# Optimization experiments

Measured on AMD Instinct MI355X. Metric: run time of the kernel, lower is better.

The kernel has to match this reference:

```python
import jax, jax.numpy as jnp
import numpy as np

EPS = 1e-5
LEAK = 0.33  # scn LeakyReLU default leakiness


def leaky(x):
    return jnp.where(x > 0, x, LEAK * x)


def subm_conv(feat, idx, mask, w):
    # feat: [N,C], idx: [N,K] int, mask: [N,K] bool, w: [K,Cin,Cout]
    g = feat[idx] * mask[..., None]          # [N,K,C] gather of active neighbors
    return jnp.einsum('nkc,kcd->nd', g, w)   # [N,Cout]


def batch_norm(x, gamma, beta):
    # scn BatchNormalization in training mode: batch stats over active sites
    m = x.mean(axis=0)
    v = x.var(axis=0)
    return (x - m) * jax.lax.rsqrt(v + EPS) * gamma + beta


def setup_inputs() -> dict:
    key = jax.random.key(0)
    ks = jax.random.split(key, 8)
    N, K, C, B = 131072, 9, 64, 4
    features = jax.random.normal(ks[0], (N, C), dtype=jnp.float32)
    neighbor_idx = jax.random.randint(ks[1], (N, K), 0, N, dtype=jnp.int32)
    # center offset always points at self (submanifold conv semantics)
    neighbor_idx = neighbor_idx.at[:, K // 2].set(jnp.arange(N, dtype=jnp.int32))
    neighbor_mask = jax.random.randint(ks[2], (N, K), 0, 2) > 0
    neighbor_mask = neighbor_mask.at[:, K // 2].set(True)
    scale = 1.0 / np.sqrt(K * C)
    conv1_w = jax.random.normal(ks[3], (B, K, C, C), dtype=jnp.float32) * scale
    conv2_w = jax.random.normal(ks[4], (B, K, C, C), dtype=jnp.float32) * scale
    bn1_gamma = jnp.ones((B, C), dtype=jnp.float32)
    bn1_beta = jnp.zeros((B, C), dtype=jnp.float32)
    bn2_gamma = jnp.ones((B, C), dtype=jnp.float32)
    bn2_beta = jnp.zeros((B, C), dtype=jnp.float32)
    return {
        'features': features, 'neighbor_idx': neighbor_idx, 'neighbor_mask': neighbor_mask,
        'conv1_w': conv1_w, 'bn1_gamma': bn1_gamma, 'bn1_beta': bn1_beta,
        'conv2_w': conv2_w, 'bn2_gamma': bn2_gamma, 'bn2_beta': bn2_beta,
    }


def reference(features, neighbor_idx, neighbor_mask, conv1_w, bn1_gamma, bn1_beta,
              conv2_w, bn2_gamma, bn2_beta):
    x = features
    n_blocks = conv1_w.shape[0]
    for b in range(n_blocks):
        residual = x
        out = subm_conv(x, neighbor_idx, neighbor_mask, conv1_w[b])
        out = leaky(batch_norm(out, bn1_gamma[b], bn1_beta[b]))
        out = subm_conv(out, neighbor_idx, neighbor_mask, conv2_w[b])
        out = batch_norm(out, bn2_gamma[b], bn2_beta[b])
        x = leaky(out + residual)
    return x
```

## Files before the change

kernel.cpp:

```cpp
#include <hip/hip_runtime.h>
#include <hip/hip_bf16.h>
#include <stdint.h>

#define NROWS 131072
#define EPSBN 1e-5f
#define LEAKK 0.33f
#define NCOPY 8

typedef __bf16 bf16x8_t __attribute__((ext_vector_type(8)));
typedef float  f32x4_t  __attribute__((ext_vector_type(4)));

__device__ __forceinline__ float leaky_f(float x) { return fmaxf(x, LEAKK * x); }

#define GLDS16(g, l)                                                          \
    __builtin_amdgcn_global_load_lds(                                         \
        (const __attribute__((address_space(1))) void*)(g),                   \
        (__attribute__((address_space(3))) void*)(l), 16, 0, 0)

#define CFENCE() asm volatile("" ::: "memory")

__global__ __launch_bounds__(256, 4) void conv_kernel(
    const __bf16* __restrict__ src,
    const int* __restrict__ cidxT,
    const __bf16* __restrict__ wt,
    __bf16* __restrict__ dst,
    float* __restrict__ stat_out)
{
    __shared__ char Bw[2][8192];

    const int tid  = threadIdx.x;
    const int lane = tid & 63;
    const int wv   = tid >> 6;
    const int quad = lane >> 4;
    const int l15  = lane & 15;
    const int row0 = blockIdx.x << 7;
    const int srow = tid >> 3;
    const int cg   = (tid & 7) ^ (srow & 7);
    const int ldsl = (tid & 192) << 4;
    const int sxor = l15 & 7;

    const char* srcb = (const char*)src;
    const char* wtb  = (const char*)wt;

    f32x4_t acc[2][4];
#pragma unroll
    for (int mt = 0; mt < 2; ++mt)
#pragma unroll
        for (int nt = 0; nt < 4; ++nt)
            acc[mt][nt] = (f32x4_t){0.f, 0.f, 0.f, 0.f};

    const int ibase = row0 + (wv << 5) + l15;
    const unsigned qofs = (unsigned)(quad << 4);

    int ixv[2][2];
#pragma unroll
    for (int mt = 0; mt < 2; ++mt) ixv[0][mt] = cidxT[ibase + (mt << 4)];
#pragma unroll
    for (int mt = 0; mt < 2; ++mt) ixv[1][mt] = cidxT[NROWS + ibase + (mt << 4)];
    CFENCE();
#pragma unroll
    for (int i = 0; i < 2; ++i)
        GLDS16(wtb + (((i << 5) + srow) << 7) + (cg << 4),
               &Bw[0][(i << 12) + ldsl]);
    CFENCE();
    bf16x8_t areg[2][2][2];
#pragma unroll
    for (int mt = 0; mt < 2; ++mt) {
        unsigned vo = ((unsigned)ixv[0][mt] << 7) + qofs;
#pragma unroll
        for (int ks = 0; ks < 2; ++ks)
            areg[0][mt][ks] = *(const bf16x8_t*)(srcb + vo + (ks << 6));
    }
    CFENCE();

#pragma unroll
    for (int k = 0; k < 9; ++k) {
        if (k < 7) {
#pragma unroll
            for (int mt = 0; mt < 2; ++mt)
                ixv[k & 1][mt] = cidxT[(k + 2) * NROWS + ibase + (mt << 4)];
        }
        CFENCE();
        if (k < 8) {
#pragma unroll
            for (int i = 0; i < 2; ++i)
                GLDS16(wtb + ((size_t)(k + 1) << 13)
                           + (((i << 5) + srow) << 7) + (cg << 4),
                       &Bw[(k + 1) & 1][(i << 12) + ldsl]);
        }
        CFENCE();
        if (k < 8) {
#pragma unroll
            for (int mt = 0; mt < 2; ++mt) {
                unsigned vo = ((unsigned)ixv[(k + 1) & 1][mt] << 7) + qofs;
#pragma unroll
                for (int ks = 0; ks < 2; ++ks)
                    areg[(k + 1) & 1][mt][ks] =
                        *(const bf16x8_t*)(srcb + vo + (ks << 6));
            }
        }
        CFENCE();
        if (k < 7)       asm volatile("s_waitcnt vmcnt(12)" ::: "memory");
        else if (k == 7) asm volatile("s_waitcnt vmcnt(10)" ::: "memory");
        else             asm volatile("s_waitcnt vmcnt(4)"  ::: "memory");
        __builtin_amdgcn_s_barrier();
        bf16x8_t bq[4][2];
#pragma unroll
        for (int ks = 0; ks < 2; ++ks) {
            const int slot = ((quad | (ks << 2)) ^ sxor) << 4;
#pragma unroll
            for (int nt = 0; nt < 4; ++nt)
                bq[nt][ks] = *(const bf16x8_t*)
                    &Bw[k & 1][(((nt << 4) + l15) << 7) + slot];
        }
        __builtin_amdgcn_s_setprio(1);
#pragma unroll
        for (int ks = 0; ks < 2; ++ks)
#pragma unroll
            for (int mt = 0; mt < 2; ++mt)
#pragma unroll
                for (int nt = 0; nt < 4; ++nt)
                    acc[mt][nt] = __builtin_amdgcn_mfma_f32_16x16x32_bf16(
                        areg[k & 1][mt][ks], bq[nt][ks], acc[mt][nt], 0, 0, 0);
        __builtin_amdgcn_s_setprio(0);
        CFENCE();
        asm volatile("s_waitcnt lgkmcnt(0)" ::: "memory");
        __builtin_amdgcn_s_barrier();
        CFENCE();
    }

#pragma unroll
    for (int mt = 0; mt < 2; ++mt) {
        int rowb = row0 + (wv << 5) + (mt << 4) + (quad << 2);
#pragma unroll
        for (int nt = 0; nt < 4; ++nt) {
            int col = (nt << 4) + l15;
#pragma unroll
            for (int r = 0; r < 4; ++r)
                dst[((size_t)(rowb + r) << 6) + col] = (__bf16)acc[mt][nt][r];
        }
    }
    float* red = (float*)Bw;
    __syncthreads();
    if (tid < 128) red[tid] = 0.f;
    __syncthreads();
#pragma unroll
    for (int nt = 0; nt < 4; ++nt) {
        float s = 0.f, q = 0.f;
#pragma unroll
        for (int mt = 0; mt < 2; ++mt)
#pragma unroll
            for (int r = 0; r < 4; ++r) { float v = acc[mt][nt][r]; s += v; q += v * v; }
        s += __shfl_xor(s, 16); s += __shfl_xor(s, 32);
        q += __shfl_xor(q, 16); q += __shfl_xor(q, 32);
        if (lane < 16) {
            atomicAdd(&red[(nt << 4) + lane], s);
            atomicAdd(&red[64 + (nt << 4) + lane], q);
        }
    }
    __syncthreads();
    if (tid < 128)
        atomicAdd(&stat_out[((blockIdx.x & (NCOPY - 1)) << 7) + tid], red[tid]);
}

__global__ __launch_bounds__(256) void bnact_kernel(
    __bf16* __restrict__ y, const float* __restrict__ stat,
    const float* __restrict__ gamma, const float* __restrict__ beta)
{
    __shared__ float sc[64], sh[64];
    int tid = threadIdx.x;
    if (tid < 128) {
        float s = 0.f;
#pragma unroll
        for (int c = 0; c < NCOPY; ++c) s += stat[(c << 7) + tid];
        ((float*)sc)[tid >= 64 ? 0 : 0] = 0.f;
        if (tid < 64) sc[tid] = s;
        else          sh[tid - 64] = s;
    }
    __syncthreads();
    if (tid < 64) {
        float m = sc[tid] * (1.f / NROWS);
        float v = sh[tid] * (1.f / NROWS) - m * m;
        float s = gamma[tid] * rsqrtf(v + EPSBN);
        sc[tid] = s;
        sh[tid] = beta[tid] - m * s;
    }
    __syncthreads();
    size_t base = ((((size_t)blockIdx.x << 8) | tid) << 3);
    int c0 = (int)(base & 63);
    bf16x8_t hv = *(bf16x8_t*)(y + base);
#pragma unroll
    for (int j = 0; j < 8; ++j) {
        float f = (float)hv[j];
        f = leaky_f(f * sc[c0 + j] + sh[c0 + j]);
        hv[j] = (__bf16)f;
    }
    *(bf16x8_t*)(y + base) = hv;
}

__global__ __launch_bounds__(256) void resid_kernel(
    const __bf16* __restrict__ z, const float* __restrict__ featin,
    __bf16* __restrict__ xh, float* __restrict__ dout,
    const float* __restrict__ stat, const float* __restrict__ gamma,
    const float* __restrict__ beta, int isfirst, int isfinal)
{
    __shared__ float sc[64], sh[64];
    int tid = threadIdx.x;
    if (tid < 128) {
        float s = 0.f;
#pragma unroll
        for (int c = 0; c < NCOPY; ++c) s += stat[(c << 7) + tid];
        if (tid < 64) sc[tid] = s;
        else          sh[tid - 64] = s;
    }
    __syncthreads();
    if (tid < 64) {
        float m = sc[tid] * (1.f / NROWS);
        float v = sh[tid] * (1.f / NROWS) - m * m;
        float s = gamma[tid] * rsqrtf(v + EPSBN);
        sc[tid] = s;
        sh[tid] = beta[tid] - m * s;
    }
    __syncthreads();
    size_t base = ((((size_t)blockIdx.x << 8) | tid) << 3);
    int c0 = (int)(base & 63);
    bf16x8_t zv = *(const bf16x8_t*)(z + base);
    float xv[8];
    if (isfirst) {
        float4 xa = *(const float4*)(featin + base);
        float4 xb = *(const float4*)(featin + base + 4);
#pragma unroll
        for (int j = 0; j < 4; ++j) { xv[j] = (&xa.x)[j]; xv[4 + j] = (&xb.x)[j]; }
    } else {
        bf16x8_t xr = *(const bf16x8_t*)(xh + base);
#pragma unroll
        for (int j = 0; j < 8; ++j) xv[j] = (float)xr[j];
    }
    float o[8];
#pragma unroll
    for (int j = 0; j < 8; ++j)
        o[j] = leaky_f((float)zv[j] * sc[c0 + j] + sh[c0 + j] + xv[j]);
    if (isfinal) {
        *(float4*)(dout + base)     = make_float4(o[0], o[1], o[2], o[3]);
        *(float4*)(dout + base + 4) = make_float4(o[4], o[5], o[6], o[7]);
    } else {
        bf16x8_t h;
#pragma unroll
        for (int j = 0; j < 8; ++j) h[j] = (__bf16)o[j];
        *(bf16x8_t*)(xh + base) = h;
    }
}

__global__ __launch_bounds__(256) void prep_kernel(
    const float* __restrict__ feat, const float* __restrict__ w1,
    const float* __restrict__ w2, const int* __restrict__ nidx,
    const unsigned char* __restrict__ mraw,
    __bf16* __restrict__ fh, __bf16* __restrict__ yh,
    __bf16* __restrict__ wtp, int* __restrict__ cidxT,
    float* __restrict__ stats)
{
    size_t t = ((size_t)blockIdx.x << 8) | threadIdx.x;
    if (t < 8192) stats[t] = 0.f;
    if (t < 64) {
        fh[(size_t)NROWS * 64 + t] = (__bf16)0.f;
        yh[(size_t)NROWS * 64 + t] = (__bf16)0.f;
    }
    if (t < 1048576) {
        size_t i = t << 3;
        float4 a = *(const float4*)(feat + i);
        float4 b = *(const float4*)(feat + i + 4);
        bf16x8_t h;
        h[0] = (__bf16)a.x; h[1] = (__bf16)a.y; h[2] = (__bf16)a.z; h[3] = (__bf16)a.w;
        h[4] = (__bf16)b.x; h[5] = (__bf16)b.y; h[6] = (__bf16)b.z; h[7] = (__bf16)b.w;
        *(bf16x8_t*)(fh + i) = h;
    }
    if (t < 294912) {
        int o = (int)t;
        int c = o & 63, d = (o >> 6) & 63;
        int kk = o >> 12;
        int k = kk % 9, bb = (kk / 9) & 3, cv = kk / 36;
        const float* w = cv ? w2 : w1;
        float v = w[((size_t)((bb * 9 + k) * 64 + c) << 6) + d];
        wtp[o] = (__bf16)v;
    }
    if (t < NROWS) {
        int n = (int)t;
        bool benc = (mraw[13] != 0);
        const unsigned int* mw = (const unsigned int*)mraw;
#pragma unroll
        for (int j = 0; j < 9; ++j) {
            int e = n * 9 + j;
            bool m = benc ? (mraw[e] != 0) : (mw[e] != 0u);
            cidxT[j * NROWS + n] = m ? nidx[e] : NROWS;
        }
    }
}

extern "C" void kernel_launch(void* const* d_in, const int* in_sizes, int n_in,
                              void* d_out, int out_size, void* d_ws, size_t ws_size,
                              hipStream_t stream) {
    const float* feat = (const float*)d_in[0];
    const int* nidx = (const int*)d_in[1];
    const unsigned char* mraw = (const unsigned char*)d_in[2];
    const float* w1 = (const float*)d_in[3];
    const float* g1 = (const float*)d_in[4];
    const float* b1 = (const float*)d_in[5];
    const float* w2 = (const float*)d_in[6];
    const float* g2 = (const float*)d_in[7];
    const float* b2 = (const float*)d_in[8];
    float* out = (float*)d_out;

    char* ws = (char*)d_ws;
    __bf16* xh    = (__bf16*)ws;
    __bf16* yh    = (__bf16*)(ws + 17825792);
    __bf16* zh    = (__bf16*)(ws + 35651584);
    __bf16* wtp   = (__bf16*)(ws + 53477376);
    float*  stats = (float*)(ws + 54525952);
    int*    cidxT = (int*)(ws + 54591488);

    prep_kernel<<<4096, 256, 0, stream>>>(feat, w1, w2, nidx, mraw,
                                          xh, yh, wtp, cidxT, stats);

    for (int b = 0; b < 4; ++b) {
        conv_kernel<<<1024, 256, 0, stream>>>(
            xh, cidxT, wtp + (size_t)b * 9 * 4096,
            yh, stats + (size_t)(2 * b) * 1024);
        bnact_kernel<<<4096, 256, 0, stream>>>(
            yh, stats + (size_t)(2 * b) * 1024, g1 + b * 64, b1 + b * 64);
        conv_kernel<<<1024, 256, 0, stream>>>(
            yh, cidxT, wtp + (size_t)(4 + b) * 9 * 4096,
            zh, stats + (size_t)(2 * b + 1) * 1024);
        resid_kernel<<<4096, 256, 0, stream>>>(
            zh, feat, xh, out,
            stats + (size_t)(2 * b + 1) * 1024, g2 + b * 64, b2 + b * 64,
            (b == 0) ? 1 : 0, (b == 3) ? 1 : 0);
    }
}
```

Before: 355.4 us.

## Fuse BN1+LeakyReLU into second conv's gather prologue

Removes the standalone bnact kernel, which read and rewrote the whole intermediate activation. BN1 scale and shift plus LeakyReLU are now applied inside the second conv kernel to each gathered neighbor fragment before the MFMA. Masked (sentinel) neighbors are zeroed after the transform so padding stays zero. This saves one full read-write pass over the activations and one launch per block. The cost is repeated elementwise BN work on every gathered row (9x redundancy) plus extra per-iteration LDS reads of the scale/shift vectors.

```diff
diff --git a/kernel.cpp b/kernel.cpp
--- a/kernel.cpp
+++ b/kernel.cpp
@@ -18,6 +18,7 @@
         (__attribute__((address_space(3))) void*)(l), 16, 0, 0)
 
 #define CFENCE() asm volatile("" ::: "memory")
+
 
 __global__ __launch_bounds__(256, 4) void conv_kernel(
     const __bf16* __restrict__ src,
@@ -163,39 +164,203 @@
         atomicAdd(&stat_out[((blockIdx.x & (NCOPY - 1)) << 7) + tid], red[tid]);
 }
 
-__global__ __launch_bounds__(256) void bnact_kernel(
-    __bf16* __restrict__ y, const float* __restrict__ stat,
+__global__ __launch_bounds__(256, 4) void convbn_kernel(
+    const __bf16* __restrict__ src,
+    const int* __restrict__ cidxT,
+    const __bf16* __restrict__ wt,
+    __bf16* __restrict__ dst,
+    float* __restrict__ stat_out,
+    const float* __restrict__ stat_in,
     const float* __restrict__ gamma, const float* __restrict__ beta)
 {
-    __shared__ float sc[64], sh[64];
-    int tid = threadIdx.x;
+    __shared__ char Bw[2][8192];
+    __shared__ float scsh[128];
+    __shared__ float scD[64], shD[64];
+
+    const int tid  = threadIdx.x;
+    const int lane = tid & 63;
+    const int wv   = tid >> 6;
+    const int quad = lane >> 4;
+    const int l15  = lane & 15;
+    const int row0 = blockIdx.x << 7;
+    const int srow = tid >> 3;
+    const int cg   = (tid & 7) ^ (srow & 7);
+    const int ldsl = (tid & 192) << 4;
+    const int sxor = l15 & 7;
+
+    const char* srcb = (const char*)src;
+    const char* wtb  = (const char*)wt;
+
+    f32x4_t acc[2][4];
+#pragma unroll
+    for (int mt = 0; mt < 2; ++mt)
+#pragma unroll
+        for (int nt = 0; nt < 4; ++nt)
+            acc[mt][nt] = (f32x4_t){0.f, 0.f, 0.f, 0.f};
+
+    const int ibase = row0 + (wv << 5) + l15;
+    const unsigned qofs = (unsigned)(quad << 4);
+
+    int ixv[2][2], ixs[2][2];
+#pragma unroll
+    for (int mt = 0; mt < 2; ++mt) ixv[0][mt] = cidxT[ibase + (mt << 4)];
+#pragma unroll
+    for (int mt = 0; mt < 2; ++mt) ixv[1][mt] = cidxT[NROWS + ibase + (mt << 4)];
+    CFENCE();
+#pragma unroll
+    for (int i = 0; i < 2; ++i)
+        GLDS16(wtb + (((i << 5) + srow) << 7) + (cg << 4),
+               &Bw[0][(i << 12) + ldsl]);
+    CFENCE();
     if (tid < 128) {
         float s = 0.f;
 #pragma unroll
-        for (int c = 0; c < NCOPY; ++c) s += stat[(c << 7) + tid];
-        ((float*)sc)[tid >= 64 ? 0 : 0] = 0.f;
-        if (tid < 64) sc[tid] = s;
-        else          sh[tid - 64] = s;
+        for (int c = 0; c < NCOPY; ++c) s += stat_in[(c << 7) + tid];
+        scsh[tid] = s;
     }
     __syncthreads();
     if (tid < 64) {
-        float m = sc[tid] * (1.f / NROWS);
-        float v = sh[tid] * (1.f / NROWS) - m * m;
+        float m = scsh[tid] * (1.f / NROWS);
+        float v = scsh[64 + tid] * (1.f / NROWS) - m * m;
         float s = gamma[tid] * rsqrtf(v + EPSBN);
-        sc[tid] = s;
-        sh[tid] = beta[tid] - m * s;
-    }
-    __syncthreads();
-    size_t base = ((((size_t)blockIdx.x << 8) | tid) << 3);
-    int c0 = (int)(base & 63);
-    bf16x8_t hv = *(bf16x8_t*)(y + base);
-#pragma unroll
-    for (int j = 0; j < 8; ++j) {
-        float f = (float)hv[j];
-        f = leaky_f(f * sc[c0 + j] + sh[c0 + j]);
-        hv[j] = (__bf16)f;
-    }
-    *(bf16x8_t*)(y + base) = hv;
+        scD[tid] = s;
+        shD[tid] = beta[tid] - m * s;
+    }
+    __syncthreads();
+    asm volatile("s_waitcnt vmcnt(0)" ::: "memory");
+    __builtin_amdgcn_s_barrier();
+    CFENCE();
+
+    bf16x8_t areg[2][2][2];
+#pragma unroll
+    for (int mt = 0; mt < 2; ++mt) {
+        ixs[0][mt] = ixv[0][mt];
+        unsigned vo = ((unsigned)ixv[0][mt] << 7) + qofs;
+#pragma unroll
+        for (int ks = 0; ks < 2; ++ks)
+            areg[0][mt][ks] = *(const bf16x8_t*)(srcb + vo + (ks << 6));
+    }
+    CFENCE();
+
+#pragma unroll
+    for (int k = 0; k < 9; ++k) {
+        if (k < 7) {
+#pragma unroll
+            for (int mt = 0; mt < 2; ++mt)
+                ixv[k & 1][mt] = cidxT[(k + 2) * NROWS + ibase + (mt << 4)];
+        }
+        CFENCE();
+        if (k < 8) {
+#pragma unroll
+            for (int i = 0; i < 2; ++i)
+                GLDS16(wtb + ((size_t)(k + 1) << 13)
+                           + (((i << 5) + srow) << 7) + (cg << 4),
+                       &Bw[(k + 1) & 1][(i << 12) + ldsl]);
+        }
+        CFENCE();
+        if (k < 8) {
+#pragma unroll
+            for (int mt = 0; mt < 2; ++mt) {
+                int ix = ixv[(k + 1) & 1][mt];
+                ixs[(k + 1) & 1][mt] = ix;
+                unsigned vo = ((unsigned)ix << 7) + qofs;
+#pragma unroll
+                for (int ks = 0; ks < 2; ++ks)
+                    areg[(k + 1) & 1][mt][ks] =
+                        *(const bf16x8_t*)(srcb + vo + (ks << 6));
+            }
+        }
+        CFENCE();
+        if (k < 7)       asm volatile("s_waitcnt vmcnt(12)" ::: "memory");
+        else if (k == 7) asm volatile("s_waitcnt vmcnt(10)" ::: "memory");
+        else             asm volatile("s_waitcnt vmcnt(4)"  ::: "memory");
+        __builtin_amdgcn_s_barrier();
+        f32x4_t scq[2][2], shq[2][2];
+#pragma unroll
+        for (int ks = 0; ks < 2; ++ks) {
+            int cb = (ks << 5) + (quad << 3);
+            scq[ks][0] = *(const f32x4_t*)&scD[cb];
+            scq[ks][1] = *(const f32x4_t*)&scD[cb + 4];
+            shq[ks][0] = *(const f32x4_t*)&shD[cb];
+            shq[ks][1] = *(const f32x4_t*)&shD[cb + 4];
+        }
+        bf16x8_t ta[2][2];
+        const bf16x8_t zfrag = {};
+#pragma unroll
+        for (int mt = 0; mt < 2; ++mt) {
+            bool dead = (ixs[k & 1][mt] == NROWS);
+#pragma unroll
+            for (int ks = 0; ks < 2; ++ks) {
+                bf16x8_t a = areg[k & 1][mt][ks];
+                bf16x8_t t;
+#pragma unroll
+                for (int j = 0; j < 8; ++j) {
+                    float f = (float)a[j];
+                    float y = fmaf(scq[ks][j >> 2][j & 3], f,
+                                   shq[ks][j >> 2][j & 3]);
+                    y = fmaxf(y, LEAKK * y);
+                    t[j] = (__bf16)y;
+                }
+                ta[mt][ks] = dead ? zfrag : t;
+            }
+        }
+        bf16x8_t bq[4][2];
+#pragma unroll
+        for (int ks = 0; ks < 2; ++ks) {
+            const int slot = ((quad | (ks << 2)) ^ sxor) << 4;
+#pragma unroll
+            for (int nt = 0; nt < 4; ++nt)
+                bq[nt][ks] = *(const bf16x8_t*)
+                    &Bw[k & 1][(((nt << 4) + l15) << 7) + slot];
+        }
+        __builtin_amdgcn_s_setprio(1);
+#pragma unroll
+        for (int ks = 0; ks < 2; ++ks)
+#pragma unroll
+            for (int mt = 0; mt < 2; ++mt)
+#pragma unroll
+                for (int nt = 0; nt < 4; ++nt)
+                    acc[mt][nt] = __builtin_amdgcn_mfma_f32_16x16x32_bf16(
+                        ta[mt][ks], bq[nt][ks], acc[mt][nt], 0, 0, 0);
+        __builtin_amdgcn_s_setprio(0);
+        CFENCE();
+        asm volatile("s_waitcnt lgkmcnt(0)" ::: "memory");
+        __builtin_amdgcn_s_barrier();
+        CFENCE();
+    }
+
+#pragma unroll
+    for (int mt = 0; mt < 2; ++mt) {
+        int rowb = row0 + (wv << 5) + (mt << 4) + (quad << 2);
+#pragma unroll
+        for (int nt = 0; nt < 4; ++nt) {
+            int col = (nt << 4) + l15;
+#pragma unroll
+            for (int r = 0; r < 4; ++r)
+                dst[((size_t)(rowb + r) << 6) + col] = (__bf16)acc[mt][nt][r];
+        }
+    }
+    float* red = (float*)Bw;
+    __syncthreads();
+    if (tid < 128) red[tid] = 0.f;
+    __syncthreads();
+#pragma unroll
+    for (int nt = 0; nt < 4; ++nt) {
+        float s = 0.f, q = 0.f;
+#pragma unroll
+        for (int mt = 0; mt < 2; ++mt)
+#pragma unroll
+            for (int r = 0; r < 4; ++r) { float v = acc[mt][nt][r]; s += v; q += v * v; }
+        s += __shfl_xor(s, 16); s += __shfl_xor(s, 32);
+        q += __shfl_xor(q, 16); q += __shfl_xor(q, 32);
+        if (lane < 16) {
+            atomicAdd(&red[(nt << 4) + lane], s);
+            atomicAdd(&red[64 + (nt << 4) + lane], q);
+        }
+    }
+    __syncthreads();
+    if (tid < 128)
+        atomicAdd(&stat_out[((blockIdx.x & (NCOPY - 1)) << 7) + tid], red[tid]);
 }
 
 __global__ __launch_bounds__(256) void resid_kernel(
@@ -325,11 +490,10 @@
         conv_kernel<<<1024, 256, 0, stream>>>(
             xh, cidxT, wtp + (size_t)b * 9 * 4096,
             yh, stats + (size_t)(2 * b) * 1024);
-        bnact_kernel<<<4096, 256, 0, stream>>>(
-            yh, stats + (size_t)(2 * b) * 1024, g1 + b * 64, b1 + b * 64);
-        conv_kernel<<<1024, 256, 0, stream>>>(
+        convbn_kernel<<<1024, 256, 0, stream>>>(
             yh, cidxT, wtp + (size_t)(4 + b) * 9 * 4096,
-            zh, stats + (size_t)(2 * b + 1) * 1024);
+            zh, stats + (size_t)(2 * b + 1) * 1024,
+            stats + (size_t)(2 * b) * 1024, g1 + b * 64, b1 + b * 64);
         resid_kernel<<<4096, 256, 0, stream>>>(
             zh, feat, xh, out,
             stats + (size_t)(2 * b + 1) * 1024, g2 + b * 64, b2 + b * 64,
```

Result: faster. 335.6 us (-5.5%).
